# Optimization experiments

Measured on AMD Instinct MI355X. Metric: run time of the kernel, lower is better.

## Reference

```python
import jax, jax.numpy as jnp
import numpy as np

HIDDEN = 1024
HEADS = 16
HEAD_DIM = HIDDEN // HEADS
B, S = 2, 2048


def setup_inputs() -> dict:
    key = jax.random.key(0)
    k1, k2, k3 = jax.random.split(key, 3)
    x = jax.random.normal(k1, (B, S, HIDDEN), dtype=jnp.float32)
    qkv_w = jax.random.normal(k2, (3 * HIDDEN, HIDDEN), dtype=jnp.float32) * (HIDDEN ** -0.5)
    out_w = jax.random.normal(k3, (HIDDEN, HIDDEN), dtype=jnp.float32) * (HIDDEN ** -0.5)
    return {"x": x, "qkv_w": qkv_w, "out_w": out_w}


def reference(x, qkv_w, out_w):
    b, s, d = x.shape
    scale = HEAD_DIM ** -0.5
    # qkv projection (Linear without bias: x @ W^T)
    qkv = x @ qkv_w.T                                   # [b, s, 3d]
    qkv = qkv.reshape(b, s, 3, HEADS, HEAD_DIM)
    qkv = jnp.transpose(qkv, (2, 0, 3, 1, 4))           # [3, b, h, s, hd]
    q, k, v = qkv[0] * scale, qkv[1], qkv[2]
    # causal attention (blocked torch loop == full causal softmax attention)
    scores = jnp.einsum('bhqd,bhkd->bhqk', q, k)        # [b, h, s, s]
    causal = jnp.tril(jnp.ones((s, s), dtype=bool))
    scores = jnp.where(causal[None, None], scores, -jnp.inf)
    weights = jax.nn.softmax(scores, axis=-1)
    attn = jnp.einsum('bhqk,bhkd->bhqd', weights, v)    # [b, h, s, hd]
    attn = jnp.transpose(attn, (0, 2, 1, 3)).reshape(b, s, d)
    return attn @ out_w.T
```

## Files before the change

### kernel.cpp

```cpp
#include <hip/hip_runtime.h>
#include <hip/hip_bf16.h>
#include <math.h>

#define HIDDEN 1024
#define HEADS 16
#define HDIM 64
#define BATCH 2
#define SEQ 2048
#define BHN (BATCH*HEADS)
#define MTOT (BATCH*SEQ)

typedef __attribute__((ext_vector_type(8))) short short8;
typedef __attribute__((ext_vector_type(4))) short short4v;
typedef __attribute__((ext_vector_type(4))) float floatx4;

#define GL2LDS(gsrc, ldst) __builtin_amdgcn_global_load_lds( \
    (const __attribute__((address_space(1))) void*)(gsrc), \
    (__attribute__((address_space(3))) void*)(ldst), 16, 0, 0)

__device__ __forceinline__ short f2bf(float f) {
  union { float f; unsigned u; } v; v.f = f;
  unsigned u = v.u;
  unsigned r = (u + 0x7fffu + ((u >> 16) & 1u)) >> 16;
  return (short)r;
}

__global__ __launch_bounds__(256) void cvt3_f32_bf16(
    const float* __restrict__ a, const float* __restrict__ b, const float* __restrict__ c,
    short* __restrict__ oa, short* __restrict__ ob, short* __restrict__ oc) {
  int i = blockIdx.x * 256 + threadIdx.x;
  const float* src; short* dst; int j;
  if (i < 1048576)      { src = a; dst = oa; j = i; }
  else if (i < 1835008) { src = b; dst = ob; j = i - 1048576; }
  else                  { src = c; dst = oc; j = i - 1835008; }
  float4 f = reinterpret_cast<const float4*>(src)[j];
  short4 o;
  o.x = f2bf(f.x); o.y = f2bf(f.y); o.z = f2bf(f.z); o.w = f2bf(f.w);
  reinterpret_cast<short4*>(dst)[j] = o;
}

template<int EPI, int BN>
__global__ __launch_bounds__(256) void gemm_bt(
    const short* __restrict__ A, const short* __restrict__ B,
    int M, int N, int K,
    float* __restrict__ outF,
    short* __restrict__ outQ, short* __restrict__ outK, short* __restrict__ outV)
{
  constexpr int WN = BN / 2;
  constexpr int NI = BN / 32;
  __shared__ __align__(16) short As[128*32];
  __shared__ __align__(16) short Bs[BN*32];
  const int tid = threadIdx.x;
  const int wv = tid >> 6;
  const int lane = tid & 63;
  const int l15 = lane & 15;
  const int quad = lane >> 4;
  const int wm = wv >> 1, wn = wv & 1;
  const int row0 = blockIdx.y * 128, col0 = blockIdx.x * BN;

  floatx4 acc[4][NI];
#pragma unroll
  for (int i = 0; i < 4; i++)
#pragma unroll
    for (int j = 0; j < NI; j++) acc[i][j] = (floatx4){0.f, 0.f, 0.f, 0.f};

  for (int k0 = 0; k0 < K; k0 += 32) {
#pragma unroll
    for (int rd = 0; rd < 2; ++rd) {
      int chunk = rd * 256 + tid;
      int r = chunk >> 2, c = (chunk & 3) << 3;
      GL2LDS(A + (long)(row0 + r) * K + k0 + c, As + (rd * 256 + wv * 64) * 8);
    }
#pragma unroll
    for (int rd = 0; rd < BN / 64; ++rd) {
      int chunk = rd * 256 + tid;
      int r = chunk >> 2, c = (chunk & 3) << 3;
      GL2LDS(B + (long)(col0 + r) * K + k0 + c, Bs + (rd * 256 + wv * 64) * 8);
    }
    __syncthreads();

    short8 af[4], bfr[NI];
#pragma unroll
    for (int mi = 0; mi < 4; mi++)
      af[mi] = *(const short8*)(As + (wm * 64 + mi * 16 + l15) * 32 + quad * 8);
#pragma unroll
    for (int ni = 0; ni < NI; ni++)
      bfr[ni] = *(const short8*)(Bs + (wn * WN + ni * 16 + l15) * 32 + quad * 8);
#pragma unroll
    for (int mi = 0; mi < 4; mi++)
#pragma unroll
      for (int ni = 0; ni < NI; ni++)
        acc[mi][ni] = __builtin_amdgcn_mfma_f32_16x16x32_bf16(af[mi], bfr[ni], acc[mi][ni], 0, 0, 0);
    __syncthreads();
  }

  if (EPI == 2) {
#pragma unroll
    for (int mi = 0; mi < 4; mi++) {
      int rr = row0 + wm * 64 + mi * 16 + quad * 4;
#pragma unroll
      for (int ni = 0; ni < NI; ni++) {
        int cc = col0 + wn * WN + ni * 16 + l15;
#pragma unroll
        for (int r = 0; r < 4; r++)
          outF[(long)(rr + r) * N + cc] = acc[mi][ni][r];
      }
    }
  } else {
#pragma unroll
    for (int mi = 0; mi < 4; mi++) {
      int rowg = row0 + wm * 64 + mi * 16 + quad * 4;
#pragma unroll
      for (int ni = 0; ni < NI; ni++) {
        int j = col0 + wn * WN + ni * 16 + l15;
        int t = j >> 10;
        int rem = j & 1023;
        int h = rem >> 6, d = rem & 63;
#pragma unroll
        for (int r = 0; r < 4; r++) {
          int i = rowg + r;
          int b = i >> 11, s = i & 2047;
          int bh = b * HEADS + h;
          float v = acc[mi][ni][r];
          if (t == 0)      outQ[(bh * SEQ + s) * HDIM + d] = f2bf(v * 0.18033688011112042f);
          else if (t == 1) outK[(bh * SEQ + s) * HDIM + d] = f2bf(v);
          else             outV[(bh * HDIM + d) * SEQ + s] = f2bf(v);
        }
      }
    }
  }
}

__device__ __forceinline__ void stage_kv(const short* __restrict__ kg,
                                         const short* __restrict__ vT,
                                         int bh, int kt, short* KsB, short* VsB,
                                         int tid, int wv) {
#pragma unroll
  for (int i = 0; i < 2; ++i) {
    int slot = i * 256 + tid;
    int r = slot >> 3;
    int sc = ((slot & 7) ^ (r & 7)) << 3;
    GL2LDS(kg + (bh * SEQ + kt * 64 + r) * HDIM + sc, KsB + (i * 256 + wv * 64) * 8);
    GL2LDS(vT + (bh * HDIM + r) * SEQ + kt * 64 + sc, VsB + (i * 256 + wv * 64) * 8);
  }
}

__global__ __launch_bounds__(256, 3) void flash_attn(
    const short* __restrict__ qg, const short* __restrict__ kg,
    const short* __restrict__ vT, short* __restrict__ attn)
{
  __shared__ __align__(16) short Ks[2][64 * 64];
  __shared__ __align__(16) short Vs[2][64 * 64];

  const int tid = threadIdx.x;
  const int wv = tid >> 6, lane = tid & 63;
  const int l15 = lane & 15, quad = lane >> 4;
  const int bh = blockIdx.y;
  const int t = (bh < 16) ? (15 - (int)blockIdx.x) : (int)blockIdx.x;
  const int m0 = t * 128 + wv * 32;
  const int swl = l15 & 7;

  short8 aq[2][2];
#pragma unroll
  for (int mi = 0; mi < 2; mi++) {
    const short* qp = qg + (long)(bh * SEQ + m0 + mi * 16 + l15) * HDIM + quad * 8;
    aq[mi][0] = *(const short8*)qp;
    aq[mi][1] = *(const short8*)(qp + 32);
  }

  const short ONE = (short)0x3F80;
  const short4v ones4 = {ONE, ONE, ONE, ONE};

  floatx4 o[2][4], lsum[2];
#pragma unroll
  for (int mi = 0; mi < 2; mi++) {
    lsum[mi] = (floatx4){0.f, 0.f, 0.f, 0.f};
#pragma unroll
    for (int nt = 0; nt < 4; nt++) o[mi][nt] = (floatx4){0.f, 0.f, 0.f, 0.f};
  }

  const int ntiles = 2 * t + 2;
  stage_kv(kg, vT, bh, 0, Ks[0], Vs[0], tid, wv);

  for (int kt = 0; kt < ntiles; ++kt) {
    __syncthreads();
    const int buf = kt & 1;
    if (kt + 1 < ntiles)
      stage_kv(kg, vT, bh, kt + 1, Ks[buf ^ 1], Vs[buf ^ 1], tid, wv);

    if (kt * 64 <= m0 + 31) {
      const short* KsB = Ks[buf];
      const short* VsB = Vs[buf];

      floatx4 sc[2][4];
#pragma unroll
      for (int mi = 0; mi < 2; mi++)
#pragma unroll
        for (int nh = 0; nh < 4; nh++) sc[mi][nh] = (floatx4){0.f, 0.f, 0.f, 0.f};
#pragma unroll
      for (int nh = 0; nh < 4; nh++) {
        const short* kp = KsB + (nh * 16 + l15) * 64;
        short8 kf0 = *(const short8*)(kp + ((quad ^ swl) << 3));
        short8 kf1 = *(const short8*)(kp + (((4 + quad) ^ swl) << 3));
#pragma unroll
        for (int mi = 0; mi < 2; mi++) {
          sc[mi][nh] = __builtin_amdgcn_mfma_f32_16x16x32_bf16(kf0, aq[mi][0], sc[mi][nh], 0, 0, 0);
          sc[mi][nh] = __builtin_amdgcn_mfma_f32_16x16x32_bf16(kf1, aq[mi][1], sc[mi][nh], 0, 0, 0);
        }
      }

      short4v pa[2][4];
#pragma unroll
      for (int mi = 0; mi < 2; mi++) {
        const int qrow = m0 + mi * 16 + l15;
        const bool full = (kt * 64 + 63) <= (m0 + mi * 16);
#pragma unroll
        for (int nh = 0; nh < 4; nh++) {
          unsigned u[4];
#pragma unroll
          for (int r = 0; r < 4; r++) {
            float pe = __builtin_amdgcn_exp2f(sc[mi][nh][r]);
            if (!full) {
              const int kpos = kt * 64 + nh * 16 + quad * 4 + r;
              pe = (kpos <= qrow) ? pe : 0.f;
            }
            u[r] = __builtin_bit_cast(unsigned, pe) & 0xffff0000u;
          }
          uint2 w;
          w.x = (u[0] >> 16) | u[1];
          w.y = (u[2] >> 16) | u[3];
          pa[mi][nh] = __builtin_bit_cast(short4v, w);
        }
      }

#pragma unroll
      for (int kk = 0; kk < 4; kk++) {
        short4v bv[4];
#pragma unroll
        for (int nt = 0; nt < 4; nt++) {
          const int ch = (kk * 2 + (quad >> 1)) ^ swl;
          bv[nt] = *(const short4v*)(VsB + (nt * 16 + l15) * 64 + (ch << 3) + ((quad & 1) << 2));
        }
#pragma unroll
        for (int mi = 0; mi < 2; mi++) {
          lsum[mi] = __builtin_amdgcn_mfma_f32_16x16x16bf16_1k(pa[mi][kk], ones4, lsum[mi], 0, 0, 0);
#pragma unroll
          for (int nt = 0; nt < 4; nt++)
            o[mi][nt] = __builtin_amdgcn_mfma_f32_16x16x16bf16_1k(pa[mi][kk], bv[nt], o[mi][nt], 0, 0, 0);
        }
      }
    }
  }

  const int b = bh >> 4, h = bh & 15;
#pragma unroll
  for (int mi = 0; mi < 2; mi++)
#pragma unroll
    for (int r = 0; r < 4; r++) {
      const float inv = 1.0f / lsum[mi][r];
      const int s = m0 + mi * 16 + quad * 4 + r;
#pragma unroll
      for (int nt = 0; nt < 4; nt++)
        attn[(long)(b * SEQ + s) * HIDDEN + h * HDIM + nt * 16 + l15] = f2bf(o[mi][nt][r] * inv);
    }
}

extern "C" void kernel_launch(void* const* d_in, const int* in_sizes, int n_in,
                              void* d_out, int out_size, void* d_ws, size_t ws_size,
                              hipStream_t stream) {
  const float* x     = (const float*)d_in[0];
  const float* qkv_w = (const float*)d_in[1];
  const float* out_w = (const float*)d_in[2];
  float* out = (float*)d_out;

  short* xb   = (short*)d_ws;
  short* wqb  = xb  + MTOT * HIDDEN;
  short* wob  = wqb + 3 * HIDDEN * HIDDEN;
  short* qB   = wob + HIDDEN * HIDDEN;
  short* kB   = qB  + BHN * SEQ * HDIM;
  short* vTB  = kB  + BHN * SEQ * HDIM;
  short* attn = vTB + BHN * SEQ * HDIM;

  cvt3_f32_bf16<<<dim3(8192), dim3(256), 0, stream>>>(x, qkv_w, out_w, xb, wqb, wob);

  gemm_bt<1, 128><<<dim3(3 * HIDDEN / 128, MTOT / 128), dim3(256), 0, stream>>>(
      xb, wqb, MTOT, 3 * HIDDEN, HIDDEN, nullptr, qB, kB, vTB);

  flash_attn<<<dim3(SEQ / 128, BHN), dim3(256), 0, stream>>>(qB, kB, vTB, attn);

  gemm_bt<2, 64><<<dim3(HIDDEN / 64, MTOT / 128), dim3(256), 0, stream>>>(
      attn, wob, MTOT, HIDDEN, HIDDEN, out, nullptr, nullptr, nullptr);
}
```

Before: 199.8 us.

## Deepen GEMM K-tile with swizzled LDS and shrink attention blocks to 64 rows

The GEMM now stages 64-wide K slices into XOR-swizzled shared memory and issues two MFMAs per fragment pair. This halves the number of barrier/load iterations and avoids bank conflicts on the wider rows. Flash attention switches to 128-thread blocks covering 64 query rows, with a grid ordered heads-first and longest tiles first. That removes the per-wave skip branch and evens out causal load imbalance, at the cost of less K/V reuse per block and more blocks.

```diff
diff --git a/kernel.cpp b/kernel.cpp
--- a/kernel.cpp
+++ b/kernel.cpp
@@ -48,13 +48,14 @@
 {
   constexpr int WN = BN / 2;
   constexpr int NI = BN / 32;
-  __shared__ __align__(16) short As[128*32];
-  __shared__ __align__(16) short Bs[BN*32];
+  __shared__ __align__(16) short As[128*64];
+  __shared__ __align__(16) short Bs[BN*64];
   const int tid = threadIdx.x;
   const int wv = tid >> 6;
   const int lane = tid & 63;
   const int l15 = lane & 15;
   const int quad = lane >> 4;
+  const int swl = l15 & 7;
   const int wm = wv >> 1, wn = wv & 1;
   const int row0 = blockIdx.y * 128, col0 = blockIdx.x * BN;
 
@@ -64,33 +65,43 @@
 #pragma unroll
     for (int j = 0; j < NI; j++) acc[i][j] = (floatx4){0.f, 0.f, 0.f, 0.f};
 
-  for (int k0 = 0; k0 < K; k0 += 32) {
-#pragma unroll
-    for (int rd = 0; rd < 2; ++rd) {
+  for (int k0 = 0; k0 < K; k0 += 64) {
+#pragma unroll
+    for (int rd = 0; rd < 4; ++rd) {
       int chunk = rd * 256 + tid;
-      int r = chunk >> 2, c = (chunk & 3) << 3;
+      int r = chunk >> 3, c = ((chunk & 7) ^ (r & 7)) << 3;
       GL2LDS(A + (long)(row0 + r) * K + k0 + c, As + (rd * 256 + wv * 64) * 8);
     }
 #pragma unroll
-    for (int rd = 0; rd < BN / 64; ++rd) {
+    for (int rd = 0; rd < BN / 32; ++rd) {
       int chunk = rd * 256 + tid;
-      int r = chunk >> 2, c = (chunk & 3) << 3;
+      int r = chunk >> 3, c = ((chunk & 7) ^ (r & 7)) << 3;
       GL2LDS(B + (long)(col0 + r) * K + k0 + c, Bs + (rd * 256 + wv * 64) * 8);
     }
     __syncthreads();
 
-    short8 af[4], bfr[NI];
+    short8 af[4][2], bfr[NI][2];
+#pragma unroll
+    for (int mi = 0; mi < 4; mi++) {
+      const short* ap = As + (wm * 64 + mi * 16 + l15) * 64;
+#pragma unroll
+      for (int kk = 0; kk < 2; kk++)
+        af[mi][kk] = *(const short8*)(ap + (((kk * 4 + quad) ^ swl) << 3));
+    }
+#pragma unroll
+    for (int ni = 0; ni < NI; ni++) {
+      const short* bp = Bs + (wn * WN + ni * 16 + l15) * 64;
+#pragma unroll
+      for (int kk = 0; kk < 2; kk++)
+        bfr[ni][kk] = *(const short8*)(bp + (((kk * 4 + quad) ^ swl) << 3));
+    }
 #pragma unroll
     for (int mi = 0; mi < 4; mi++)
-      af[mi] = *(const short8*)(As + (wm * 64 + mi * 16 + l15) * 32 + quad * 8);
-#pragma unroll
-    for (int ni = 0; ni < NI; ni++)
-      bfr[ni] = *(const short8*)(Bs + (wn * WN + ni * 16 + l15) * 32 + quad * 8);
-#pragma unroll
-    for (int mi = 0; mi < 4; mi++)
 #pragma unroll
       for (int ni = 0; ni < NI; ni++)
-        acc[mi][ni] = __builtin_amdgcn_mfma_f32_16x16x32_bf16(af[mi], bfr[ni], acc[mi][ni], 0, 0, 0);
+#pragma unroll
+        for (int kk = 0; kk < 2; kk++)
+          acc[mi][ni] = __builtin_amdgcn_mfma_f32_16x16x32_bf16(af[mi][kk], bfr[ni][kk], acc[mi][ni], 0, 0, 0);
     __syncthreads();
   }
 
@@ -136,16 +147,16 @@
                                          int bh, int kt, short* KsB, short* VsB,
                                          int tid, int wv) {
 #pragma unroll
-  for (int i = 0; i < 2; ++i) {
-    int slot = i * 256 + tid;
+  for (int i = 0; i < 4; ++i) {
+    int slot = i * 128 + tid;
     int r = slot >> 3;
     int sc = ((slot & 7) ^ (r & 7)) << 3;
-    GL2LDS(kg + (bh * SEQ + kt * 64 + r) * HDIM + sc, KsB + (i * 256 + wv * 64) * 8);
-    GL2LDS(vT + (bh * HDIM + r) * SEQ + kt * 64 + sc, VsB + (i * 256 + wv * 64) * 8);
-  }
-}
-
-__global__ __launch_bounds__(256, 3) void flash_attn(
+    GL2LDS(kg + (bh * SEQ + kt * 64 + r) * HDIM + sc, KsB + (i * 128 + wv * 64) * 8);
+    GL2LDS(vT + (bh * HDIM + r) * SEQ + kt * 64 + sc, VsB + (i * 128 + wv * 64) * 8);
+  }
+}
+
+__global__ __launch_bounds__(128, 2) void flash_attn(
     const short* __restrict__ qg, const short* __restrict__ kg,
     const short* __restrict__ vT, short* __restrict__ attn)
 {
@@ -155,9 +166,9 @@
   const int tid = threadIdx.x;
   const int wv = tid >> 6, lane = tid & 63;
   const int l15 = lane & 15, quad = lane >> 4;
-  const int bh = blockIdx.y;
-  const int t = (bh < 16) ? (15 - (int)blockIdx.x) : (int)blockIdx.x;
-  const int m0 = t * 128 + wv * 32;
+  const int bh = blockIdx.x;
+  const int rt = 31 - (int)blockIdx.y;
+  const int m0 = rt * 64 + wv * 32;
   const int swl = l15 & 7;
 
   short8 aq[2][2];
@@ -179,7 +190,7 @@
     for (int nt = 0; nt < 4; nt++) o[mi][nt] = (floatx4){0.f, 0.f, 0.f, 0.f};
   }
 
-  const int ntiles = 2 * t + 2;
+  const int ntiles = rt + 1;
   stage_kv(kg, vT, bh, 0, Ks[0], Vs[0], tid, wv);
 
   for (int kt = 0; kt < ntiles; ++kt) {
@@ -188,66 +199,64 @@
     if (kt + 1 < ntiles)
       stage_kv(kg, vT, bh, kt + 1, Ks[buf ^ 1], Vs[buf ^ 1], tid, wv);
 
-    if (kt * 64 <= m0 + 31) {
-      const short* KsB = Ks[buf];
-      const short* VsB = Vs[buf];
-
-      floatx4 sc[2][4];
-#pragma unroll
-      for (int mi = 0; mi < 2; mi++)
-#pragma unroll
-        for (int nh = 0; nh < 4; nh++) sc[mi][nh] = (floatx4){0.f, 0.f, 0.f, 0.f};
+    const short* KsB = Ks[buf];
+    const short* VsB = Vs[buf];
+
+    floatx4 sc[2][4];
+#pragma unroll
+    for (int mi = 0; mi < 2; mi++)
+#pragma unroll
+      for (int nh = 0; nh < 4; nh++) sc[mi][nh] = (floatx4){0.f, 0.f, 0.f, 0.f};
+#pragma unroll
+    for (int nh = 0; nh < 4; nh++) {
+      const short* kp = KsB + (nh * 16 + l15) * 64;
+      short8 kf0 = *(const short8*)(kp + ((quad ^ swl) << 3));
+      short8 kf1 = *(const short8*)(kp + (((4 + quad) ^ swl) << 3));
+#pragma unroll
+      for (int mi = 0; mi < 2; mi++) {
+        sc[mi][nh] = __builtin_amdgcn_mfma_f32_16x16x32_bf16(kf0, aq[mi][0], sc[mi][nh], 0, 0, 0);
+        sc[mi][nh] = __builtin_amdgcn_mfma_f32_16x16x32_bf16(kf1, aq[mi][1], sc[mi][nh], 0, 0, 0);
+      }
+    }
+
+    short4v pa[2][4];
+#pragma unroll
+    for (int mi = 0; mi < 2; mi++) {
+      const int qrow = m0 + mi * 16 + l15;
+      const bool full = (kt * 64 + 63) <= (m0 + mi * 16);
 #pragma unroll
       for (int nh = 0; nh < 4; nh++) {
-        const short* kp = KsB + (nh * 16 + l15) * 64;
-        short8 kf0 = *(const short8*)(kp + ((quad ^ swl) << 3));
-        short8 kf1 = *(const short8*)(kp + (((4 + quad) ^ swl) << 3));
-#pragma unroll
-        for (int mi = 0; mi < 2; mi++) {
-          sc[mi][nh] = __builtin_amdgcn_mfma_f32_16x16x32_bf16(kf0, aq[mi][0], sc[mi][nh], 0, 0, 0);
-          sc[mi][nh] = __builtin_amdgcn_mfma_f32_16x16x32_bf16(kf1, aq[mi][1], sc[mi][nh], 0, 0, 0);
+        unsigned u[4];
+#pragma unroll
+        for (int r = 0; r < 4; r++) {
+          float pe = __builtin_amdgcn_exp2f(sc[mi][nh][r]);
+          if (!full) {
+            const int kpos = kt * 64 + nh * 16 + quad * 4 + r;
+            pe = (kpos <= qrow) ? pe : 0.f;
+          }
+          u[r] = __builtin_bit_cast(unsigned, pe) & 0xffff0000u;
         }
-      }
-
-      short4v pa[2][4];
+        uint2 w;
+        w.x = (u[0] >> 16) | u[1];
+        w.y = (u[2] >> 16) | u[3];
+        pa[mi][nh] = __builtin_bit_cast(short4v, w);
+      }
+    }
+
+#pragma unroll
+    for (int kk = 0; kk < 4; kk++) {
+      short4v bv[4];
+#pragma unroll
+      for (int nt = 0; nt < 4; nt++) {
+        const int ch = (kk * 2 + (quad >> 1)) ^ swl;
+        bv[nt] = *(const short4v*)(VsB + (nt * 16 + l15) * 64 + (ch << 3) + ((quad & 1) << 2));
+      }
 #pragma unroll
       for (int mi = 0; mi < 2; mi++) {
-        const int qrow = m0 + mi * 16 + l15;
-        const bool full = (kt * 64 + 63) <= (m0 + mi * 16);
-#pragma unroll
-        for (int nh = 0; nh < 4; nh++) {
-          unsigned u[4];
-#pragma unroll
-          for (int r = 0; r < 4; r++) {
-            float pe = __builtin_amdgcn_exp2f(sc[mi][nh][r]);
-            if (!full) {
-              const int kpos = kt * 64 + nh * 16 + quad * 4 + r;
-              pe = (kpos <= qrow) ? pe : 0.f;
-            }
-            u[r] = __builtin_bit_cast(unsigned, pe) & 0xffff0000u;
-          }
-          uint2 w;
-          w.x = (u[0] >> 16) | u[1];
-          w.y = (u[2] >> 16) | u[3];
-          pa[mi][nh] = __builtin_bit_cast(short4v, w);
-        }
-      }
-
-#pragma unroll
-      for (int kk = 0; kk < 4; kk++) {
-        short4v bv[4];
-#pragma unroll
-        for (int nt = 0; nt < 4; nt++) {
-          const int ch = (kk * 2 + (quad >> 1)) ^ swl;
-          bv[nt] = *(const short4v*)(VsB + (nt * 16 + l15) * 64 + (ch << 3) + ((quad & 1) << 2));
-        }
-#pragma unroll
-        for (int mi = 0; mi < 2; mi++) {
-          lsum[mi] = __builtin_amdgcn_mfma_f32_16x16x16bf16_1k(pa[mi][kk], ones4, lsum[mi], 0, 0, 0);
-#pragma unroll
-          for (int nt = 0; nt < 4; nt++)
-            o[mi][nt] = __builtin_amdgcn_mfma_f32_16x16x16bf16_1k(pa[mi][kk], bv[nt], o[mi][nt], 0, 0, 0);
-        }
+        lsum[mi] = __builtin_amdgcn_mfma_f32_16x16x16bf16_1k(pa[mi][kk], ones4, lsum[mi], 0, 0, 0);
+#pragma unroll
+        for (int nt = 0; nt < 4; nt++)
+          o[mi][nt] = __builtin_amdgcn_mfma_f32_16x16x16bf16_1k(pa[mi][kk], bv[nt], o[mi][nt], 0, 0, 0);
       }
     }
   }
@@ -286,7 +295,7 @@
   gemm_bt<1, 128><<<dim3(3 * HIDDEN / 128, MTOT / 128), dim3(256), 0, stream>>>(
       xb, wqb, MTOT, 3 * HIDDEN, HIDDEN, nullptr, qB, kB, vTB);
 
-  flash_attn<<<dim3(SEQ / 128, BHN), dim3(256), 0, stream>>>(qB, kB, vTB, attn);
+  flash_attn<<<dim3(BHN, SEQ / 64), dim3(128), 0, stream>>>(qB, kB, vTB, attn);
 
   gemm_bt<2, 64><<<dim3(HIDDEN / 64, MTOT / 128), dim3(256), 0, stream>>>(
       attn, wob, MTOT, HIDDEN, HIDDEN, out, nullptr, nullptr, nullptr);
```

Measured after the change: 180.4 us. 9.7% less time.
